# Kernel optimization log

Hardware: AMD Instinct MI355X
Metric: run time of the kernel (lower is better)

## Reference

```python
import math
import jax, jax.numpy as jnp
import numpy as np

B, T, S, C, E = 16, 1024, 1024, 1024, 1024
NORM_C = 0.5


def setup_inputs() -> dict:
    key = jax.random.key(0)
    ks = jax.random.split(key, 9)
    return {
        "x": jax.random.normal(ks[0], (B, T, C), dtype=jnp.float32),
        "target_embedding": jax.random.normal(ks[1], (B, T, E), dtype=jnp.float32),
        "enc_keys": jax.random.normal(ks[2], (B, E, S), dtype=jnp.float32),      # encoder_out[0]
        "enc_values": jax.random.normal(ks[3], (B, S, E), dtype=jnp.float32),    # encoder_out[1]
        "encoder_padding_mask": jax.random.randint(ks[4], (B, S), 0, 2).astype(bool),
        "w_in": jax.random.normal(ks[5], (E, C), dtype=jnp.float32) / np.sqrt(C),
        "b_in": jnp.zeros((E,), dtype=jnp.float32),
        "w_out": jax.random.normal(ks[6], (C, E), dtype=jnp.float32) / np.sqrt(E),
        "b_out": jnp.zeros((C,), dtype=jnp.float32),
    }


def reference(x, target_embedding, enc_keys, enc_values, encoder_padding_mask,
              w_in, b_in, w_out, b_out):
    scale = jnp.float32(math.sqrt(NORM_C))
    residual = x
    # in_projection + target embedding, rescale
    h = (jnp.einsum("btc,ec->bte", x, w_in) + b_in + target_embedding) * scale
    # attention scores: bmm with keys [B,E,S]
    scores = jnp.einsum("bte,bes->bts", h, enc_keys)
    neg_inf = jnp.float32(float("-inf"))
    scores = jnp.where(encoder_padding_mask[:, None, :], neg_inf, scores)
    attn_scores = jax.nn.softmax(scores, axis=-1)
    # weighted sum of values
    ctx = jnp.einsum("bts,bse->bte", attn_scores, enc_values)
    # data-dependent rescale: multiply by sqrt(valid token count)
    s = jnp.float32(S) - jnp.sum(encoder_padding_mask.astype(ctx.dtype), axis=1, keepdims=True)  # [B,1]
    s = s[:, :, None]  # [B,1,1]
    ctx = ctx * (s * jax.lax.rsqrt(s))
    out = (jnp.einsum("bte,ce->btc", ctx, w_out) + b_out + residual) * scale
    return (out, attn_scores)
```

## Files before the change

### kernel.cpp

```cpp
#include <hip/hip_runtime.h>


#define SCALE_F 0.70710678118654752440f

constexpr int BB = 16, TT = 1024, SS = 1024, CC = 1024, EE = 1024;

typedef float    f32x4 __attribute__((ext_vector_type(4)));
typedef _Float16 f16x8 __attribute__((ext_vector_type(8)));
typedef _Float16 f16x4 __attribute__((ext_vector_type(4)));

__device__ __forceinline__ void gload_lds16(const _Float16* g, _Float16* l) {
  __builtin_amdgcn_global_load_lds((const __attribute__((address_space(1))) void*)g,
                                   (__attribute__((address_space(3))) void*)l,
                                   16, 0, 0);
}

#define VMCNT(N) asm volatile("s_waitcnt vmcnt(" #N ")" ::: "memory")
#define LGKM(N)  asm volatile("s_waitcnt lgkmcnt(" #N ")" ::: "memory")
#define SBAR()   asm volatile("s_barrier" ::: "memory")
#define DSR(dst, a, off) \
  asm volatile("ds_read_b128 %0, %1 offset:" #off : "=v"(dst) : "v"(a))

__global__ __launch_bounds__(256) void cvt_f16(const float* __restrict__ s,
                                               _Float16* __restrict__ d, long n) {
  long i = ((long)blockIdx.x * 256 + threadIdx.x) * 8;
  if (i >= n) return;
  f32x4 a = *(const f32x4*)(s + i);
  f32x4 b = *(const f32x4*)(s + i + 4);
  f16x8 h;
  h[0]=(_Float16)a[0]; h[1]=(_Float16)a[1]; h[2]=(_Float16)a[2]; h[3]=(_Float16)a[3];
  h[4]=(_Float16)b[0]; h[5]=(_Float16)b[1]; h[6]=(_Float16)b[2]; h[7]=(_Float16)b[3];
  *(f16x8*)(d + i) = h;
}

__global__ __launch_bounds__(256) void transpose_cvt(const float* __restrict__ src,
                                                     _Float16* __restrict__ dst,
                                                     int R, int Cc) {
  __shared__ float tile[64][65];
  const int b = blockIdx.z;
  const int r0 = blockIdx.y * 64, c0 = blockIdx.x * 64;
  const int t = threadIdx.x;
  const int tr = t >> 4, tc4 = (t & 15) * 4;
  const float* s = src + (size_t)b * R * Cc;
#pragma unroll
  for (int i = 0; i < 4; ++i) {
    f32x4 v = *(const f32x4*)(s + (size_t)(r0 + i * 16 + tr) * Cc + c0 + tc4);
    tile[i * 16 + tr][tc4 + 0] = v[0]; tile[i * 16 + tr][tc4 + 1] = v[1];
    tile[i * 16 + tr][tc4 + 2] = v[2]; tile[i * 16 + tr][tc4 + 3] = v[3];
  }
  __syncthreads();
  _Float16* d = dst + (size_t)b * Cc * R;
#pragma unroll
  for (int j = 0; j < 4; ++j) {
    const int cl = j * 16 + tr;
    f16x4 h;
    h[0] = (_Float16)tile[tc4 + 0][cl]; h[1] = (_Float16)tile[tc4 + 1][cl];
    h[2] = (_Float16)tile[tc4 + 2][cl]; h[3] = (_Float16)tile[tc4 + 3][cl];
    *(f16x4*)(d + (size_t)(c0 + cl) * R + r0 + tc4) = h;
  }
}

__global__ __launch_bounds__(256) void mask_prep(const unsigned char* __restrict__ mraw,
                                                 float* __restrict__ maskneg,
                                                 float* __restrict__ sscale) {
  const int b = blockIdx.x, t = threadIdx.x;
  __shared__ int bytemode_sh, cnt_sh;
  if (t == 0) { bytemode_sh = 0; cnt_sh = 0; }
  __syncthreads();
  const unsigned int* mu = (const unsigned int*)mraw;
  int local = 0;
  for (int i = t; i < (BB * SS) / 4; i += 256) {
    unsigned int v = mu[i];
    if (v != 0u && v != 1u && v != 0x3f800000u) local = 1;
  }
  if (local) atomicOr(&bytemode_sh, 1);
  __syncthreads();
  const int bytemode = bytemode_sh;
  int cnt = 0;
  for (int s = t; s < SS; s += 256) {
    int m = bytemode ? (mraw[b * SS + s] != 0) : (mu[b * SS + s] != 0u);
    maskneg[b * SS + s] = m ? -__builtin_inff() : 0.0f;
    cnt += m;
  }
#pragma unroll
  for (int o = 32; o; o >>= 1) cnt += __shfl_down(cnt, o);
  if ((t & 63) == 0) atomicAdd(&cnt_sh, cnt);
  __syncthreads();
  if (t == 0) {
    float sv = (float)SS - (float)cnt_sh;
    sscale[b] = sv * rsqrtf(sv);
  }
}

template <int EPI>
__global__ __launch_bounds__(512, 2)
void gemm256(const _Float16* __restrict__ A, const _Float16* __restrict__ Bmat,
             long aStride, long bStride, long oStride,
             int M, int N, int K,
             void* __restrict__ outp,
             const float* __restrict__ bias,
             const float* __restrict__ addmat,
             const float* __restrict__ extra) {
  __shared__ __attribute__((aligned(16))) _Float16 smem[65536];

  const int t = threadIdx.x;
  const int lane = t & 63;
  const int wid = t >> 6;
  const int wm = wid >> 2, wn = wid & 3;
  const int z = blockIdx.z;
  const int lo = lane & 15, hi = lane >> 4;
  const int sx = lo & 7;
  const int nt = K >> 6;

  const int gx = gridDim.x;
  const int fblk = blockIdx.x + blockIdx.y * gx;
  const int q = (gx * gridDim.y) >> 3;
  const int wg = (fblk & 7) * q + (fblk >> 3);
  const long rowBase = (long)(wg / gx) * 256;
  const long colBase = (long)(wg % gx) * 256;

  const _Float16* Ag = A + (size_t)z * aStride + rowBase * K;
  const _Float16* Bg = Bmat + (size_t)z * bStride + colBase * K;

  const int sr8 = t >> 3;
  const int srck = (((t & 7) ^ (sr8 & 7)) << 3);

  f32x4 acc[8][4] = {};

#define STAGE8(U)                                                              \
  {                                                                            \
    const int tu_ = (U);                                                       \
    _Float16* db_ = &smem[(tu_ & 1) * 32768];                                  \
    const size_t kb_ = (size_t)tu_ * 64 + srck;                                \
    _Pragma("unroll") for (int i_ = 0; i_ < 4; ++i_)                           \
      gload_lds16(Ag + (size_t)(i_ * 64 + sr8) * K + kb_,                      \
                  db_ + i_ * 4096 + t * 8);                                    \
    _Pragma("unroll") for (int i_ = 0; i_ < 4; ++i_)                           \
      gload_lds16(Bg + (size_t)(i_ * 64 + sr8) * K + kb_,                      \
                  db_ + 16384 + i_ * 4096 + t * 8);                            \
  }

  const int lds0 = (int)(size_t)&smem[0];
  const int abase = lds0 + (wm * 128 + lo) * 128 + ((hi ^ sx) << 4);
  const int bbase = lds0 + 32768 + (wn * 64 + lo) * 128 + ((hi ^ sx) << 4);

  STAGE8(0)
  STAGE8(1)
  VMCNT(8);
  SBAR();

  for (int u = 0; u < nt; ++u) {
    const int bo = (u & 1) << 16;
    const int aad = abase + bo, bad = bbase + bo;
    const int aad1 = aad ^ 64, bad1 = bad ^ 64;
    f16x8 a0[8], b0[4], a1[8], b1[4];
    DSR(a0[0], aad, 0);     DSR(a0[1], aad, 2048);  DSR(a0[2], aad, 4096);
    DSR(a0[3], aad, 6144);  DSR(a0[4], aad, 8192);  DSR(a0[5], aad, 10240);
    DSR(a0[6], aad, 12288); DSR(a0[7], aad, 14336);
    DSR(b0[0], bad, 0);     DSR(b0[1], bad, 2048);  DSR(b0[2], bad, 4096);
    DSR(b0[3], bad, 6144);
    DSR(a1[0], aad1, 0);     DSR(a1[1], aad1, 2048);  DSR(a1[2], aad1, 4096);
    DSR(a1[3], aad1, 6144);  DSR(a1[4], aad1, 8192);  DSR(a1[5], aad1, 10240);
    DSR(a1[6], aad1, 12288); DSR(a1[7], aad1, 14336);
    DSR(b1[0], bad1, 0);     DSR(b1[1], bad1, 2048);  DSR(b1[2], bad1, 4096);
    DSR(b1[3], bad1, 6144);
    LGKM(12);
    __builtin_amdgcn_sched_barrier(0);
    __builtin_amdgcn_s_setprio(1);
#pragma unroll
    for (int mi = 0; mi < 8; ++mi)
#pragma unroll
      for (int ni = 0; ni < 4; ++ni)
        acc[mi][ni] = __builtin_amdgcn_mfma_f32_16x16x32_f16(a0[mi], b0[ni],
                                                             acc[mi][ni], 0, 0, 0);
    __builtin_amdgcn_s_setprio(0);
    LGKM(0);
    __builtin_amdgcn_sched_barrier(0);
    SBAR();
    if (u + 2 < nt) STAGE8(u + 2)
    __builtin_amdgcn_s_setprio(1);
#pragma unroll
    for (int mi = 0; mi < 8; ++mi)
#pragma unroll
      for (int ni = 0; ni < 4; ++ni)
        acc[mi][ni] = __builtin_amdgcn_mfma_f32_16x16x32_f16(a1[mi], b1[ni],
                                                             acc[mi][ni], 0, 0, 0);
    __builtin_amdgcn_s_setprio(0);
    if (u + 2 < nt)       { VMCNT(8); }
    else if (u + 2 == nt) { VMCNT(0); }
    SBAR();
  }

  constexpr int EPS = 68;
  const int fr = lane & 15;
  const int fq = (lane >> 4) * 4;
  const int er = lane >> 2;
  const int ec = (lane & 3) * 16;
  const long gc0 = colBase + wn * 64 + ec;
  float* ep = (float*)smem + wid * (16 * EPS);

  f32x4 biasv[4], maskv[4], av[4];
  float sc = 0.f;
  if constexpr (EPI == 1 || EPI == 4) {
#pragma unroll
    for (int i = 0; i < 4; ++i) biasv[i] = *(const f32x4*)&bias[gc0 + i * 4];
    const long gr0 = rowBase + wm * 128 + er;
#pragma unroll
    for (int i = 0; i < 4; ++i) av[i] = *(const f32x4*)&addmat[gr0 * N + gc0 + i * 4];
  }
  if constexpr (EPI == 2) {
#pragma unroll
    for (int i = 0; i < 4; ++i) maskv[i] = *(const f32x4*)&extra[(size_t)z * N + gc0 + i * 4];
  }
  if constexpr (EPI == 3) sc = extra[z];

  __syncthreads();
#pragma unroll
  for (int mf = 0; mf < 8; ++mf) {
#pragma unroll
    for (int n = 0; n < 4; ++n)
#pragma unroll
      for (int j = 0; j < 4; ++j)
        ep[(fq + j) * EPS + n * 16 + fr] = acc[mf][n][j];
    __syncthreads();
    const long gr = rowBase + wm * 128 + mf * 16 + er;
    f32x4 r[4];
#pragma unroll
    for (int i = 0; i < 4; ++i) r[i] = *(const f32x4*)&ep[er * EPS + ec + i * 4];
    f32x4 a_cur[4];
    if constexpr (EPI == 1 || EPI == 4) {
#pragma unroll
      for (int i = 0; i < 4; ++i) a_cur[i] = av[i];
      if (mf < 7) {
        const long grn = gr + 16;
#pragma unroll
        for (int i = 0; i < 4; ++i) av[i] = *(const f32x4*)&addmat[grn * N + gc0 + i * 4];
      }
    }
    if constexpr (EPI == 1) {
      _Float16* o = (_Float16*)outp + gr * N + gc0;
#pragma unroll
      for (int g = 0; g < 2; ++g) {
        f32x4 v0 = (r[2 * g] + biasv[2 * g] + a_cur[2 * g]) * SCALE_F;
        f32x4 v1 = (r[2 * g + 1] + biasv[2 * g + 1] + a_cur[2 * g + 1]) * SCALE_F;
        f16x8 h;
        h[0]=(_Float16)v0[0]; h[1]=(_Float16)v0[1]; h[2]=(_Float16)v0[2]; h[3]=(_Float16)v0[3];
        h[4]=(_Float16)v1[0]; h[5]=(_Float16)v1[1]; h[6]=(_Float16)v1[2]; h[7]=(_Float16)v1[3];
        *(f16x8*)(o + g * 8) = h;
      }
    } else if constexpr (EPI == 2) {
      float* o = (float*)outp + (size_t)z * oStride + gr * N + gc0;
#pragma unroll
      for (int i = 0; i < 4; ++i) *(f32x4*)(o + i * 4) = r[i] + maskv[i];
    } else if constexpr (EPI == 3) {
      _Float16* o = (_Float16*)outp + (size_t)z * oStride + gr * N + gc0;
#pragma unroll
      for (int g = 0; g < 2; ++g) {
        f32x4 v0 = r[2 * g] * sc;
        f32x4 v1 = r[2 * g + 1] * sc;
        f16x8 h;
        h[0]=(_Float16)v0[0]; h[1]=(_Float16)v0[1]; h[2]=(_Float16)v0[2]; h[3]=(_Float16)v0[3];
        h[4]=(_Float16)v1[0]; h[5]=(_Float16)v1[1]; h[6]=(_Float16)v1[2]; h[7]=(_Float16)v1[3];
        *(f16x8*)(o + g * 8) = h;
      }
    } else {
      float* o = (float*)outp + gr * N + gc0;
#pragma unroll
      for (int i = 0; i < 4; ++i)
        *(f32x4*)(o + i * 4) = (r[i] + biasv[i] + a_cur[i]) * SCALE_F;
    }
    __syncthreads();
  }
}

__global__ __launch_bounds__(256) void softmax_k(float* __restrict__ attn,
                                                 _Float16* __restrict__ attn16) {
  const size_t row = blockIdx.x;
  float* p = attn + row * SS;
  const int t = threadIdx.x;
  f32x4 v = *(const f32x4*)(p + t * 4);
  __shared__ float red[8];
  float m = fmaxf(fmaxf(v[0], v[1]), fmaxf(v[2], v[3]));
#pragma unroll
  for (int o = 32; o; o >>= 1) m = fmaxf(m, __shfl_xor(m, o));
  if (!(t & 63)) red[t >> 6] = m;
  __syncthreads();
  m = fmaxf(fmaxf(red[0], red[1]), fmaxf(red[2], red[3]));
  f32x4 e;
  e[0] = __expf(v[0] - m); e[1] = __expf(v[1] - m);
  e[2] = __expf(v[2] - m); e[3] = __expf(v[3] - m);
  float s = e[0] + e[1] + e[2] + e[3];
#pragma unroll
  for (int o = 32; o; o >>= 1) s += __shfl_xor(s, o);
  if (!(t & 63)) red[4 + (t >> 6)] = s;
  __syncthreads();
  s = red[4] + red[5] + red[6] + red[7];
  const float inv = 1.0f / s;
  f32x4 o4; o4[0]=e[0]*inv; o4[1]=e[1]*inv; o4[2]=e[2]*inv; o4[3]=e[3]*inv;
  *(f32x4*)(p + t * 4) = o4;
  f16x4 h; h[0]=(_Float16)o4[0]; h[1]=(_Float16)o4[1];
  h[2]=(_Float16)o4[2]; h[3]=(_Float16)o4[3];
  *(f16x4*)(attn16 + row * SS + t * 4) = h;
}

extern "C" void kernel_launch(void* const* d_in, const int* in_sizes, int n_in,
                              void* d_out, int out_size, void* d_ws, size_t ws_size,
                              hipStream_t stream) {
  const float* x     = (const float*)d_in[0];
  const float* te    = (const float*)d_in[1];
  const float* keys  = (const float*)d_in[2];
  const float* vals  = (const float*)d_in[3];
  const void*  mask  = d_in[4];
  const float* w_in  = (const float*)d_in[5];
  const float* b_in  = (const float*)d_in[6];
  const float* w_out = (const float*)d_in[7];
  const float* b_out = (const float*)d_in[8];

  char* ws = (char*)d_ws;
  const size_t MB32 = 33554432;
  _Float16* buf0   = (_Float16*)(ws);
  _Float16* buf1   = (_Float16*)(ws + MB32);
  _Float16* keysT  = (_Float16*)(ws + 2 * MB32);
  _Float16* valsT  = (_Float16*)(ws + 3 * MB32);
  _Float16* win16  = (_Float16*)(ws + 4 * MB32);
  _Float16* wout16 = (_Float16*)(ws + 4 * MB32 + 2097152);
  float*    maskneg= (float*)   (ws + 4 * MB32 + 2 * 2097152);
  float*    sscale = (float*)   (ws + 4 * MB32 + 2 * 2097152 + 65536);

  float* out_main = (float*)d_out;
  float* attn_out = (float*)d_out + (size_t)BB * TT * CC;

  cvt_f16<<<dim3(16777216 / 2048), 256, 0, stream>>>(x, buf0, 16777216);
  cvt_f16<<<dim3(1048576 / 2048), 256, 0, stream>>>(w_in, win16, 1048576);
  cvt_f16<<<dim3(1048576 / 2048), 256, 0, stream>>>(w_out, wout16, 1048576);
  transpose_cvt<<<dim3(SS / 64, EE / 64, BB), 256, 0, stream>>>(keys, keysT, EE, SS);
  transpose_cvt<<<dim3(EE / 64, SS / 64, BB), 256, 0, stream>>>(vals, valsT, SS, EE);
  mask_prep<<<dim3(BB), 256, 0, stream>>>((const unsigned char*)mask, maskneg, sscale);

  gemm256<1><<<dim3(EE / 256, (BB * TT) / 256, 1), 512, 0, stream>>>(
      buf0, win16, 0, 0, 0, BB * TT, EE, CC, buf1, b_in, te, nullptr);
  gemm256<2><<<dim3(SS / 256, TT / 256, BB), 512, 0, stream>>>(
      buf1, keysT, (long)TT * EE, (long)SS * EE, (long)TT * SS,
      TT, SS, EE, attn_out, nullptr, nullptr, maskneg);
  softmax_k<<<dim3(BB * TT), 256, 0, stream>>>(attn_out, buf1);
  gemm256<3><<<dim3(EE / 256, TT / 256, BB), 512, 0, stream>>>(
      buf1, valsT, (long)TT * SS, (long)EE * SS, (long)TT * EE,
      TT, EE, SS, buf0, nullptr, nullptr, sscale);
  gemm256<4><<<dim3(CC / 256, (BB * TT) / 256, 1), 512, 0, stream>>>(
      buf0, wout16, 0, 0, 0, BB * TT, CC, EE, out_main, b_out, x, nullptr);
}
```

Baseline: 314.8 us.

## Fuse masked softmax into QK^T GEMM and use fp16 residual in output projection

Replaces the separate score GEMM and row-softmax kernel with one kernel. Each block computes a 64-row by full-S score tile, then applies the mask, max, exp, sum and normalise in registers, and writes both the fp32 and fp16 attention outputs directly. This removes the fp32 score round-trip through global memory. The output projection now reads the residual from the fp16 copy of x rather than fp32 x, which cuts residual traffic at some cost in precision. Buffers are reused (keysT holds the context), and the fused kernel launches only 256 large-LDS blocks, which may limit occupancy and latency hiding.

```diff
diff --git a/kernel.cpp b/kernel.cpp
--- a/kernel.cpp
+++ b/kernel.cpp
@@ -13,6 +13,11 @@
   __builtin_amdgcn_global_load_lds((const __attribute__((address_space(1))) void*)g,
                                    (__attribute__((address_space(3))) void*)l,
                                    16, 0, 0);
+}
+__device__ __forceinline__ void gload_lds4(const _Float16* g, _Float16* l) {
+  __builtin_amdgcn_global_load_lds((const __attribute__((address_space(1))) void*)g,
+                                   (__attribute__((address_space(3))) void*)l,
+                                   4, 0, 0);
 }
 
 #define VMCNT(N) asm volatile("s_waitcnt vmcnt(" #N ")" ::: "memory")
@@ -99,7 +104,7 @@
              int M, int N, int K,
              void* __restrict__ outp,
              const float* __restrict__ bias,
-             const float* __restrict__ addmat,
+             const void* __restrict__ addmat,
              const float* __restrict__ extra) {
   __shared__ __attribute__((aligned(16))) _Float16 smem[65536];
 
@@ -199,18 +204,30 @@
   const long gc0 = colBase + wn * 64 + ec;
   float* ep = (float*)smem + wid * (16 * EPS);
 
-  f32x4 biasv[4], maskv[4], av[4];
+  f32x4 biasv[4], av[4];
   float sc = 0.f;
-  if constexpr (EPI == 1 || EPI == 4) {
+  auto load_add = [&](long gr) {
+    if constexpr (EPI == 1 || EPI == 4) {
+      const float* am = (const float*)addmat;
+#pragma unroll
+      for (int i = 0; i < 4; ++i) av[i] = *(const f32x4*)&am[gr * N + gc0 + i * 4];
+    } else if constexpr (EPI == 5) {
+      const _Float16* am = (const _Float16*)addmat;
+      f16x8 h0 = *(const f16x8*)&am[gr * N + gc0];
+      f16x8 h1 = *(const f16x8*)&am[gr * N + gc0 + 8];
+#pragma unroll
+      for (int i = 0; i < 4; ++i) {
+        const f16x8& hh = i < 2 ? h0 : h1;
+        const int o = (i & 1) * 4;
+        av[i][0] = (float)hh[o]; av[i][1] = (float)hh[o + 1];
+        av[i][2] = (float)hh[o + 2]; av[i][3] = (float)hh[o + 3];
+      }
+    }
+  };
+  if constexpr (EPI == 1 || EPI == 4 || EPI == 5) {
 #pragma unroll
     for (int i = 0; i < 4; ++i) biasv[i] = *(const f32x4*)&bias[gc0 + i * 4];
-    const long gr0 = rowBase + wm * 128 + er;
-#pragma unroll
-    for (int i = 0; i < 4; ++i) av[i] = *(const f32x4*)&addmat[gr0 * N + gc0 + i * 4];
-  }
-  if constexpr (EPI == 2) {
-#pragma unroll
-    for (int i = 0; i < 4; ++i) maskv[i] = *(const f32x4*)&extra[(size_t)z * N + gc0 + i * 4];
+    load_add(rowBase + wm * 128 + er);
   }
   if constexpr (EPI == 3) sc = extra[z];
 
@@ -228,14 +245,10 @@
 #pragma unroll
     for (int i = 0; i < 4; ++i) r[i] = *(const f32x4*)&ep[er * EPS + ec + i * 4];
     f32x4 a_cur[4];
-    if constexpr (EPI == 1 || EPI == 4) {
+    if constexpr (EPI == 1 || EPI == 4 || EPI == 5) {
 #pragma unroll
       for (int i = 0; i < 4; ++i) a_cur[i] = av[i];
-      if (mf < 7) {
-        const long grn = gr + 16;
-#pragma unroll
-        for (int i = 0; i < 4; ++i) av[i] = *(const f32x4*)&addmat[grn * N + gc0 + i * 4];
-      }
+      if (mf < 7) load_add(gr + 16);
     }
     if constexpr (EPI == 1) {
       _Float16* o = (_Float16*)outp + gr * N + gc0;
@@ -248,10 +261,6 @@
         h[4]=(_Float16)v1[0]; h[5]=(_Float16)v1[1]; h[6]=(_Float16)v1[2]; h[7]=(_Float16)v1[3];
         *(f16x8*)(o + g * 8) = h;
       }
-    } else if constexpr (EPI == 2) {
-      float* o = (float*)outp + (size_t)z * oStride + gr * N + gc0;
-#pragma unroll
-      for (int i = 0; i < 4; ++i) *(f32x4*)(o + i * 4) = r[i] + maskv[i];
     } else if constexpr (EPI == 3) {
       _Float16* o = (_Float16*)outp + (size_t)z * oStride + gr * N + gc0;
 #pragma unroll
@@ -273,34 +282,208 @@
   }
 }
 
-__global__ __launch_bounds__(256) void softmax_k(float* __restrict__ attn,
-                                                 _Float16* __restrict__ attn16) {
-  const size_t row = blockIdx.x;
-  float* p = attn + row * SS;
+__global__ __launch_bounds__(512, 2)
+void gemm_sm(const _Float16* __restrict__ h16, const _Float16* __restrict__ keysT,
+             const float* __restrict__ maskneg,
+             float* __restrict__ attn, _Float16* __restrict__ attn16) {
+  __shared__ __attribute__((aligned(16))) _Float16 smem[69632];
+
   const int t = threadIdx.x;
-  f32x4 v = *(const f32x4*)(p + t * 4);
-  __shared__ float red[8];
-  float m = fmaxf(fmaxf(v[0], v[1]), fmaxf(v[2], v[3]));
-#pragma unroll
-  for (int o = 32; o; o >>= 1) m = fmaxf(m, __shfl_xor(m, o));
-  if (!(t & 63)) red[t >> 6] = m;
-  __syncthreads();
-  m = fmaxf(fmaxf(red[0], red[1]), fmaxf(red[2], red[3]));
-  f32x4 e;
-  e[0] = __expf(v[0] - m); e[1] = __expf(v[1] - m);
-  e[2] = __expf(v[2] - m); e[3] = __expf(v[3] - m);
-  float s = e[0] + e[1] + e[2] + e[3];
-#pragma unroll
-  for (int o = 32; o; o >>= 1) s += __shfl_xor(s, o);
-  if (!(t & 63)) red[4 + (t >> 6)] = s;
-  __syncthreads();
-  s = red[4] + red[5] + red[6] + red[7];
-  const float inv = 1.0f / s;
-  f32x4 o4; o4[0]=e[0]*inv; o4[1]=e[1]*inv; o4[2]=e[2]*inv; o4[3]=e[3]*inv;
-  *(f32x4*)(p + t * 4) = o4;
-  f16x4 h; h[0]=(_Float16)o4[0]; h[1]=(_Float16)o4[1];
-  h[2]=(_Float16)o4[2]; h[3]=(_Float16)o4[3];
-  *(f16x4*)(attn16 + row * SS + t * 4) = h;
+  const int lane = t & 63;
+  const int wid = t >> 6;
+  const int lo = lane & 15, hi = lane >> 4;
+
+  const int wg = ((int)blockIdx.x & 7) * 32 + ((int)blockIdx.x >> 3);
+  const int z = wg >> 4;
+  const long rowBase = (long)(wg & 15) * 64;
+
+  const _Float16* Ag = h16 + ((size_t)z * TT + rowBase) * EE;
+  const _Float16* Bg = keysT + (size_t)z * SS * EE;
+
+  const int bn_lo = t >> 2;
+  const int bslot = t & 3;
+  const int bchunk = bslot ^ (bn_lo & 3);
+  const int arow0 = t >> 4;
+  const int aslot = (t >> 2) & 3;
+  const int achunk = aslot ^ (arow0 & 3);
+  const int adw = t & 3;
+
+  f32x4 acc[4][8] = {};
+
+#define STG(U)                                                                 \
+  {                                                                            \
+    _Float16* Bb_ = &smem[((U) & 1) * 32768];                                  \
+    _Float16* Ab_ = &smem[65536 + ((U) & 1) * 2048];                           \
+    const size_t ku_ = (size_t)(U) * 32;                                       \
+    _Pragma("unroll") for (int i_ = 0; i_ < 8; ++i_) {                         \
+      const int n_ = i_ * 128 + bn_lo;                                         \
+      gload_lds16(Bg + (size_t)n_ * EE + ku_ + (bchunk << 3),                  \
+                  Bb_ + n_ * 32 + bslot * 8);                                  \
+    }                                                                          \
+    _Pragma("unroll") for (int i_ = 0; i_ < 2; ++i_) {                         \
+      const int r_ = i_ * 32 + arow0;                                          \
+      gload_lds4(Ag + (size_t)r_ * EE + ku_ + achunk * 8 + adw * 2,            \
+                 Ab_ + (i_ * 512 + t) * 2);                                    \
+    }                                                                          \
+  }
+
+  const int lds0 = (int)(size_t)&smem[0];
+  const int abase = lds0 + 131072 + lo * 64 + ((hi ^ (lo & 3)) << 4);
+  const int bbase = lds0 + wid * 8192 + lo * 64 + ((hi ^ (lo & 3)) << 4);
+
+  STG(0)
+  STG(1)
+  VMCNT(10);
+  SBAR();
+
+  for (int u = 0; u < 32; ++u) {
+    const int aad = abase + ((u & 1) << 12);
+    const int bad = bbase + ((u & 1) << 16);
+    f16x8 a[4], b[8];
+    DSR(a[0], aad, 0);    DSR(a[1], aad, 1024); DSR(a[2], aad, 2048);
+    DSR(a[3], aad, 3072);
+    DSR(b[0], bad, 0);    DSR(b[1], bad, 1024); DSR(b[2], bad, 2048);
+    DSR(b[3], bad, 3072); DSR(b[4], bad, 4096); DSR(b[5], bad, 5120);
+    DSR(b[6], bad, 6144); DSR(b[7], bad, 7168);
+    LGKM(6);
+    __builtin_amdgcn_sched_barrier(0);
+    __builtin_amdgcn_s_setprio(1);
+#pragma unroll
+    for (int ni = 0; ni < 2; ++ni)
+#pragma unroll
+      for (int mi = 0; mi < 4; ++mi)
+        acc[mi][ni] = __builtin_amdgcn_mfma_f32_16x16x32_f16(a[mi], b[ni],
+                                                             acc[mi][ni], 0, 0, 0);
+    __builtin_amdgcn_s_setprio(0);
+    LGKM(0);
+    __builtin_amdgcn_sched_barrier(0);
+    SBAR();
+    if (u + 2 < 32) STG(u + 2)
+    __builtin_amdgcn_s_setprio(1);
+#pragma unroll
+    for (int ni = 2; ni < 8; ++ni)
+#pragma unroll
+      for (int mi = 0; mi < 4; ++mi)
+        acc[mi][ni] = __builtin_amdgcn_mfma_f32_16x16x32_f16(a[mi], b[ni],
+                                                             acc[mi][ni], 0, 0, 0);
+    __builtin_amdgcn_s_setprio(0);
+    if (u + 2 < 32)       { VMCNT(10); }
+    else if (u + 2 == 32) { VMCNT(0); }
+    SBAR();
+  }
+
+  float* redm   = (float*)smem;
+  float* redf   = (float*)smem + 512;
+  float* redsum = (float*)smem + 576;
+  float* redl   = (float*)smem + 1088;
+  float* epb    = (float*)smem + 2048;
+
+  float mk[8];
+#pragma unroll
+  for (int ni = 0; ni < 8; ++ni)
+    mk[ni] = maskneg[z * SS + wid * 128 + ni * 16 + lo];
+
+  float rmax[4][4];
+#pragma unroll
+  for (int mi = 0; mi < 4; ++mi)
+#pragma unroll
+    for (int j = 0; j < 4; ++j) {
+      float v = -__builtin_inff();
+#pragma unroll
+      for (int ni = 0; ni < 8; ++ni) {
+        acc[mi][ni][j] += mk[ni];
+        v = fmaxf(v, acc[mi][ni][j]);
+      }
+#pragma unroll
+      for (int o = 1; o < 16; o <<= 1) v = fmaxf(v, __shfl_xor(v, o));
+      rmax[mi][j] = v;
+    }
+  if (lo == 0) {
+#pragma unroll
+    for (int mi = 0; mi < 4; ++mi)
+#pragma unroll
+      for (int j = 0; j < 4; ++j)
+        redm[wid * 64 + mi * 16 + hi * 4 + j] = rmax[mi][j];
+  }
+  __syncthreads();
+  if (t < 64) {
+    float m = redm[t];
+#pragma unroll
+    for (int w = 1; w < 8; ++w) m = fmaxf(m, redm[w * 64 + t]);
+    redf[t] = m;
+  }
+  __syncthreads();
+#pragma unroll
+  for (int mi = 0; mi < 4; ++mi)
+#pragma unroll
+    for (int j = 0; j < 4; ++j) {
+      const float m = redf[mi * 16 + hi * 4 + j];
+      float s = 0.f;
+#pragma unroll
+      for (int ni = 0; ni < 8; ++ni) {
+        float e = __expf(acc[mi][ni][j] - m);
+        acc[mi][ni][j] = e;
+        s += e;
+      }
+#pragma unroll
+      for (int o = 1; o < 16; o <<= 1) s += __shfl_xor(s, o);
+      rmax[mi][j] = s;
+    }
+  if (lo == 0) {
+#pragma unroll
+    for (int mi = 0; mi < 4; ++mi)
+#pragma unroll
+      for (int j = 0; j < 4; ++j)
+        redsum[wid * 64 + mi * 16 + hi * 4 + j] = rmax[mi][j];
+  }
+  __syncthreads();
+  if (t < 64) {
+    float s = redsum[t];
+#pragma unroll
+    for (int w = 1; w < 8; ++w) s += redsum[w * 64 + t];
+    redl[t] = 1.0f / s;
+  }
+  __syncthreads();
+#pragma unroll
+  for (int mi = 0; mi < 4; ++mi)
+#pragma unroll
+    for (int j = 0; j < 4; ++j) {
+      const float inv = redl[mi * 16 + hi * 4 + j];
+#pragma unroll
+      for (int ni = 0; ni < 8; ++ni) acc[mi][ni][j] *= inv;
+    }
+
+  float* ep = epb + wid * (16 * 132);
+  const int rr = lane >> 2;
+  const int cc = (lane & 3) * 32;
+#pragma unroll
+  for (int mi = 0; mi < 4; ++mi) {
+#pragma unroll
+    for (int ni = 0; ni < 8; ++ni)
+#pragma unroll
+      for (int j = 0; j < 4; ++j)
+        ep[(hi * 4 + j) * 132 + ni * 16 + lo] = acc[mi][ni][j];
+    __syncthreads();
+    f32x4 r4[8];
+#pragma unroll
+    for (int i = 0; i < 8; ++i) r4[i] = *(const f32x4*)&ep[rr * 132 + cc + i * 4];
+    const size_t base = ((size_t)z << 20) + ((size_t)(rowBase + mi * 16 + rr) << 10)
+                        + wid * 128 + cc;
+    float* ao = attn + base;
+#pragma unroll
+    for (int i = 0; i < 8; ++i) *(f32x4*)(ao + i * 4) = r4[i];
+    _Float16* ho = attn16 + base;
+#pragma unroll
+    for (int g = 0; g < 4; ++g) {
+      f16x8 h;
+      h[0]=(_Float16)r4[2*g][0]; h[1]=(_Float16)r4[2*g][1];
+      h[2]=(_Float16)r4[2*g][2]; h[3]=(_Float16)r4[2*g][3];
+      h[4]=(_Float16)r4[2*g+1][0]; h[5]=(_Float16)r4[2*g+1][1];
+      h[6]=(_Float16)r4[2*g+1][2]; h[7]=(_Float16)r4[2*g+1][3];
+      *(f16x8*)(ho + g * 8) = h;
+    }
+    __syncthreads();
+  }
 }
 
 extern "C" void kernel_launch(void* const* d_in, const int* in_sizes, int n_in,
@@ -339,13 +522,10 @@
 
   gemm256<1><<<dim3(EE / 256, (BB * TT) / 256, 1), 512, 0, stream>>>(
       buf0, win16, 0, 0, 0, BB * TT, EE, CC, buf1, b_in, te, nullptr);
-  gemm256<2><<<dim3(SS / 256, TT / 256, BB), 512, 0, stream>>>(
-      buf1, keysT, (long)TT * EE, (long)SS * EE, (long)TT * SS,
-      TT, SS, EE, attn_out, nullptr, nullptr, maskneg);
-  softmax_k<<<dim3(BB * TT), 256, 0, stream>>>(attn_out, buf1);
+  gemm_sm<<<dim3(256), 512, 0, stream>>>(buf1, keysT, maskneg, attn_out, buf1);
   gemm256<3><<<dim3(EE / 256, TT / 256, BB), 512, 0, stream>>>(
       buf1, valsT, (long)TT * SS, (long)EE * SS, (long)TT * EE,
-      TT, EE, SS, buf0, nullptr, nullptr, sscale);
-  gemm256<4><<<dim3(CC / 256, (BB * TT) / 256, 1), 512, 0, stream>>>(
-      buf0, wout16, 0, 0, 0, BB * TT, CC, EE, out_main, b_out, x, nullptr);
-}
+      TT, EE, SS, keysT, nullptr, nullptr, sscale);
+  gemm256<5><<<dim3(CC / 256, (BB * TT) / 256, 1), 512, 0, stream>>>(
+      keysT, wout16, 0, 0, 0, BB * TT, CC, EE, out_main, b_out, buf0, nullptr);
+}
```

New measurement: 318.1 us. No clear change (+1.0%).
